# Kernel tuning notes

Measured on AMD Instinct MI355X. Metric: run time of the kernel, lower is better.

The kernel has to match this reference:

```python
import jax, jax.numpy as jnp
import numpy as np

N = 65536
APP = 1024
SP = 512
HID = 512
CARD = 16
SUB = HID // CARD  # 32


def setup_inputs() -> dict:
    key = jax.random.key(0)
    ks = jax.random.split(key, 8)
    s1 = 1.0 / np.sqrt(APP)
    s2 = 1.0 / np.sqrt(SP)
    s3 = 1.0 / np.sqrt(SUB)
    return {
        "appearance": jax.random.normal(ks[0], (N, APP), jnp.float32),
        "spatial": jax.random.normal(ks[1], (N, SP), jnp.float32),
        # Batched per-branch weights (torch Linear: y = x @ W.T + b; here stored as [in, out])
        "W1": jax.random.uniform(ks[2], (CARD, APP, SUB), jnp.float32, -s1, s1),
        "b1": jax.random.uniform(ks[3], (CARD, SUB), jnp.float32, -s1, s1),
        "W2": jax.random.uniform(ks[4], (CARD, SP, SUB), jnp.float32, -s2, s2),
        "b2": jax.random.uniform(ks[5], (CARD, SP if False else SUB), jnp.float32, -s2, s2),
        "W3": jax.random.uniform(ks[6], (CARD, SUB, HID), jnp.float32, -s3, s3),
        "b3": jax.random.uniform(ks[7], (CARD, HID), jnp.float32, -s3, s3),
    }


def reference(appearance, spatial, W1, b1, W2, b2, W3, b3):
    # fc1[c] = appearance @ W1[c] + b1[c]; fc2[c] = spatial @ W2[c] + b2[c]
    h1 = jnp.einsum('na,cas->ncs', appearance, W1) + b1[None]  # [N, C, SUB]
    h2 = jnp.einsum('np,cps->ncs', spatial, W2) + b2[None]     # [N, C, SUB]
    h = jax.nn.relu(h1 + h2)
    # sum over branches of (h[:,c] @ W3[c] + b3[c]) == einsum + sum of biases
    out = jnp.einsum('ncs,csh->nh', h, W3) + jnp.sum(b3, axis=0)[None]  # [N, HID]
    return jax.nn.relu(out)
```

## Files before the change

### kernel.cpp

```cpp
#include <hip/hip_runtime.h>

typedef __attribute__((ext_vector_type(4))) float floatx4;
typedef __attribute__((ext_vector_type(8))) short bf16x8;

__device__ __forceinline__ unsigned short f2bf(float f) {
    union { float f; unsigned u; } v; v.f = f;
    unsigned r = v.u + 0x7fffu + ((v.u >> 16) & 1u);
    return (unsigned short)(r >> 16);
}

__global__ void prep_kernel(const float* __restrict__ W1, const float* __restrict__ b1,
                            const float* __restrict__ W2, const float* __restrict__ b2,
                            const float* __restrict__ W3, const float* __restrict__ b3,
                            unsigned short* __restrict__ wcat, unsigned short* __restrict__ w3f,
                            float* __restrict__ bias12, float* __restrict__ bias3s)
{
    int tid = blockIdx.x * 256 + threadIdx.x;
    if (tid < 98304) {
        int l  = tid & 63;
        int nt = (tid >> 6) & 31;
        int kc = tid >> 11;
        int n  = nt * 16 + (l & 15);
        int k0 = kc * 32 + ((l >> 4) << 3);
        int c = n >> 5, s = n & 31;
        union { unsigned short us[8]; int4 v; } pk;
        const float* src = (k0 < 1024) ? (W1 + c * 32768 + k0 * 32 + s)
                                       : (W2 + c * 16384 + (k0 - 1024) * 32 + s);
        #pragma unroll
        for (int j = 0; j < 8; ++j) pk.us[j] = f2bf(src[j * 32]);
        *(int4*)(wcat + (size_t)tid * 8) = pk.v;
    } else if (tid < 131072) {
        int t  = tid - 98304;
        int l  = t & 63;
        int nt = (t >> 6) & 31;
        int kc = t >> 11;
        int n  = nt * 16 + (l & 15);
        int k0 = kc * 32 + ((l >> 4) << 3);
        union { unsigned short us[8]; int4 v; } pk;
        const float* src = W3 + k0 * 512 + n;
        #pragma unroll
        for (int j = 0; j < 8; ++j) pk.us[j] = f2bf(src[j * 512]);
        *(int4*)(w3f + (size_t)t * 8) = pk.v;
    } else if (tid < 131584) {
        int n = tid - 131072;
        bias12[n] = b1[n] + b2[n];
        float sacc = 0.f;
        #pragma unroll
        for (int c = 0; c < 16; ++c) sacc += b3[c * 512 + n];
        bias3s[n] = sacc;
    }
}

__global__ __launch_bounds__(512, 4) void fused_main(
    const float* __restrict__ app, const float* __restrict__ sp,
    const unsigned short* __restrict__ wcat, const unsigned short* __restrict__ w3f,
    const float* __restrict__ bias12, const float* __restrict__ bias3s,
    float* __restrict__ out)
{
    __shared__ unsigned short As[2][4][64][8];
    __shared__ unsigned short Hf[4][16][64][8];

    const int tid = (int)threadIdx.x;
    const int w   = tid >> 6;
    const int l   = tid & 63;
    const int rowbase = (int)blockIdx.x * 64;

    const int sr  = tid >> 3;
    const int scc = tid & 7;
    const float* appsrc = app + (size_t)(rowbase + sr) * 1024 + scc * 4;
    const float* spsrc  = sp  + (size_t)(rowbase + sr) * 512  + scc * 4;
    unsigned short* as0 = &As[0][sr >> 4][(scc >> 1) * 16 + (sr & 15)][(scc & 1) * 4];
    unsigned short* as1 = &As[1][sr >> 4][(scc >> 1) * 16 + (sr & 15)][(scc & 1) * 4];

    floatx4 acc[4][4];
    #pragma unroll
    for (int mt = 0; mt < 4; ++mt)
        #pragma unroll
        for (int nt = 0; nt < 4; ++nt)
            acc[mt][nt] = (floatx4){0.f, 0.f, 0.f, 0.f};

    {
        float4 p = *(const float4*)(appsrc);
        union { unsigned short us[4]; int2 v; } pk;
        pk.us[0] = f2bf(p.x); pk.us[1] = f2bf(p.y);
        pk.us[2] = f2bf(p.z); pk.us[3] = f2bf(p.w);
        *(int2*)as0 = pk.v;
    }
    float4 pA = *(const float4*)(appsrc + 32);

    const unsigned short* wbase = wcat + (size_t)w * 2048 + (size_t)l * 8;
    bf16x8 bcur[4];
    #pragma unroll
    for (int nt = 0; nt < 4; ++nt)
        bcur[nt] = *(const bf16x8*)(wbase + nt * 512);

    asm volatile("s_waitcnt lgkmcnt(0)" ::: "memory");
    __builtin_amdgcn_s_barrier();
    asm volatile("" ::: "memory");

    for (int kb = 0; kb < 48; ++kb) {
        bf16x8 af[4];
        #pragma unroll
        for (int mt = 0; mt < 4; ++mt)
            af[mt] = *(const bf16x8*)(&As[kb & 1][mt][l][0]);

        float4 pB;
        if (kb + 2 < 48) {
            const float* src = (kb + 2 < 32) ? (appsrc + (kb + 2) * 32)
                                             : (spsrc + (kb - 30) * 32);
            pB = *(const float4*)src;
        }

        if (kb + 1 < 48) {
            union { unsigned short us[4]; int2 v; } pk;
            pk.us[0] = f2bf(pA.x); pk.us[1] = f2bf(pA.y);
            pk.us[2] = f2bf(pA.z); pk.us[3] = f2bf(pA.w);
            *(int2*)(((kb & 1) == 0) ? as1 : as0) = pk.v;
        }

        const unsigned short* wp = wbase + (size_t)(kb + 1) * 16384;
        #pragma unroll
        for (int nt = 0; nt < 4; ++nt) {
            #pragma unroll
            for (int mt = 0; mt < 4; ++mt)
                acc[mt][nt] = __builtin_amdgcn_mfma_f32_16x16x32_bf16(
                    af[mt], bcur[nt], acc[mt][nt], 0, 0, 0);
            if (kb + 1 < 48)
                bcur[nt] = *(const bf16x8*)(wp + nt * 512);
        }

        pA = pB;

        if (kb + 1 < 48) {
            asm volatile("s_waitcnt lgkmcnt(0)" ::: "memory");
            __builtin_amdgcn_s_barrier();
            asm volatile("" ::: "memory");
        }
    }

    const unsigned short* w3base = w3f + (size_t)w * 2048 + (size_t)l * 8;
    bf16x8 b3[4];
    #pragma unroll
    for (int nt = 0; nt < 4; ++nt)
        b3[nt] = *(const bf16x8*)(w3base + nt * 512);

    #pragma unroll
    for (int nt = 0; nt < 4; ++nt) {
        const int colg = w * 64 + nt * 16 + (l & 15);
        const float bv = bias12[colg];
        const int kc  = colg >> 5;
        const int lhi = ((colg >> 3) & 3) << 4;
        const int j   = colg & 7;
        #pragma unroll
        for (int mt = 0; mt < 4; ++mt)
            #pragma unroll
            for (int r = 0; r < 4; ++r) {
                const int rlow = ((l >> 4) << 2) + r;
                float v = acc[mt][nt][r] + bv;
                v = fmaxf(v, 0.f);
                Hf[mt][kc][lhi + rlow][j] = f2bf(v);
            }
    }
    asm volatile("s_waitcnt lgkmcnt(0)" ::: "memory");
    __builtin_amdgcn_s_barrier();
    asm volatile("" ::: "memory");

    #pragma unroll
    for (int mt = 0; mt < 4; ++mt)
        #pragma unroll
        for (int nt = 0; nt < 4; ++nt)
            acc[mt][nt] = (floatx4){0.f, 0.f, 0.f, 0.f};

    for (int kc = 0; kc < 16; ++kc) {
        bf16x8 af[4];
        #pragma unroll
        for (int mt = 0; mt < 4; ++mt)
            af[mt] = *(const bf16x8*)(&Hf[mt][kc][l][0]);
        const unsigned short* wp = w3base + (size_t)(kc + 1) * 16384;
        #pragma unroll
        for (int nt = 0; nt < 4; ++nt) {
            #pragma unroll
            for (int mt = 0; mt < 4; ++mt)
                acc[mt][nt] = __builtin_amdgcn_mfma_f32_16x16x32_bf16(
                    af[mt], b3[nt], acc[mt][nt], 0, 0, 0);
            if (kc + 1 < 16)
                b3[nt] = *(const bf16x8*)(wp + nt * 512);
        }
    }

    #pragma unroll
    for (int nt = 0; nt < 4; ++nt) {
        const int colg = w * 64 + nt * 16 + (l & 15);
        const float bv = bias3s[colg];
        #pragma unroll
        for (int mt = 0; mt < 4; ++mt)
            #pragma unroll
            for (int r = 0; r < 4; ++r) {
                const int rowg = mt * 16 + ((l >> 4) << 2) + r;
                float v = acc[mt][nt][r] + bv;
                v = fmaxf(v, 0.f);
                out[(size_t)(rowbase + rowg) * 512 + colg] = v;
            }
    }
}

extern "C" void kernel_launch(void* const* d_in, const int* in_sizes, int n_in,
                              void* d_out, int out_size, void* d_ws, size_t ws_size,
                              hipStream_t stream)
{
    const float* app = (const float*)d_in[0];
    const float* sp  = (const float*)d_in[1];
    const float* W1  = (const float*)d_in[2];
    const float* b1  = (const float*)d_in[3];
    const float* W2  = (const float*)d_in[4];
    const float* b2  = (const float*)d_in[5];
    const float* W3  = (const float*)d_in[6];
    const float* b3  = (const float*)d_in[7];

    char* ws = (char*)d_ws;
    unsigned short* wcat  = (unsigned short*)(ws);
    unsigned short* w3f   = (unsigned short*)(ws + 1572864);
    float*          b12   = (float*)(ws + 2097152);
    float*          b3s   = (float*)(ws + 2099200);

    prep_kernel<<<514, 256, 0, stream>>>(W1, b1, W2, b2, W3, b3, wcat, w3f, b12, b3s);

    float* outp = (float*)d_out;
    fused_main<<<65536 / 64, 512, 0, stream>>>(app, sp, wcat, w3f, b12, b3s, outp);
}
```

Before: 581.6 us.

## Double K-step per barrier, overlay LDS buffers, add MFMA priority hints

The main GEMM loop now handles 64 K elements per iteration instead of 32. This halves the number of block barriers, and each thread loads 8 floats per row chunk with 128-bit LDS stores. The A staging buffer and the hidden-activation buffer now share LDS through a union, which lowers the shared-memory footprint per block. Weight fragments are loaded for two K-steps at once into 8 registers, and s_setprio raises wave priority around the MFMA bursts in both GEMMs. The cost is higher register pressure and a shallower prefetch distance for the activation loads, now one iteration ahead.

```diff
diff --git a/kernel.cpp b/kernel.cpp
--- a/kernel.cpp
+++ b/kernel.cpp
@@ -57,20 +57,22 @@
     const float* __restrict__ bias12, const float* __restrict__ bias3s,
     float* __restrict__ out)
 {
-    __shared__ unsigned short As[2][4][64][8];
-    __shared__ unsigned short Hf[4][16][64][8];
+    __shared__ union {
+        unsigned short As[2][2][4][64][8];
+        unsigned short Hf[4][16][64][8];
+    } sh;
 
     const int tid = (int)threadIdx.x;
     const int w   = tid >> 6;
     const int l   = tid & 63;
     const int rowbase = (int)blockIdx.x * 64;
 
-    const int sr  = tid >> 3;
-    const int scc = tid & 7;
-    const float* appsrc = app + (size_t)(rowbase + sr) * 1024 + scc * 4;
-    const float* spsrc  = sp  + (size_t)(rowbase + sr) * 512  + scc * 4;
-    unsigned short* as0 = &As[0][sr >> 4][(scc >> 1) * 16 + (sr & 15)][(scc & 1) * 4];
-    unsigned short* as1 = &As[1][sr >> 4][(scc >> 1) * 16 + (sr & 15)][(scc & 1) * 4];
+    const int sr = tid >> 3;
+    const int kq = tid & 7;
+    const float* appsrc = app + (size_t)(rowbase + sr) * 1024 + kq * 8;
+    const float* spsrc  = sp  + (size_t)(rowbase + sr) * 512  + kq * 8;
+    unsigned short* as0 = &sh.As[0][kq >> 2][sr >> 4][(kq & 3) * 16 + (sr & 15)][0];
+    unsigned short* as1 = &sh.As[1][kq >> 2][sr >> 4][(kq & 3) * 16 + (sr & 15)][0];
 
     floatx4 acc[4][4];
     #pragma unroll
@@ -79,70 +81,79 @@
         for (int nt = 0; nt < 4; ++nt)
             acc[mt][nt] = (floatx4){0.f, 0.f, 0.f, 0.f};
 
+    const unsigned short* wbase = wcat + (size_t)w * 2048 + (size_t)l * 8;
+
+    bf16x8 bcur[8];
+    #pragma unroll
+    for (int i = 0; i < 8; ++i)
+        bcur[i] = *(const bf16x8*)(wbase + (i >> 2) * 16384 + (i & 3) * 512);
     {
-        float4 p = *(const float4*)(appsrc);
-        union { unsigned short us[4]; int2 v; } pk;
-        pk.us[0] = f2bf(p.x); pk.us[1] = f2bf(p.y);
-        pk.us[2] = f2bf(p.z); pk.us[3] = f2bf(p.w);
-        *(int2*)as0 = pk.v;
-    }
-    float4 pA = *(const float4*)(appsrc + 32);
-
-    const unsigned short* wbase = wcat + (size_t)w * 2048 + (size_t)l * 8;
-    bf16x8 bcur[4];
-    #pragma unroll
-    for (int nt = 0; nt < 4; ++nt)
-        bcur[nt] = *(const bf16x8*)(wbase + nt * 512);
-
+        float4 q0 = *(const float4*)(appsrc);
+        float4 q1 = *(const float4*)(appsrc + 4);
+        union { unsigned short us[8]; int4 v; } pk;
+        pk.us[0] = f2bf(q0.x); pk.us[1] = f2bf(q0.y); pk.us[2] = f2bf(q0.z); pk.us[3] = f2bf(q0.w);
+        pk.us[4] = f2bf(q1.x); pk.us[5] = f2bf(q1.y); pk.us[6] = f2bf(q1.z); pk.us[7] = f2bf(q1.w);
+        *(int4*)as0 = pk.v;
+    }
     asm volatile("s_waitcnt lgkmcnt(0)" ::: "memory");
     __builtin_amdgcn_s_barrier();
-    asm volatile("" ::: "memory");
-
-    for (int kb = 0; kb < 48; ++kb) {
+
+    for (int p = 0; p < 24; ++p) {
+        const int buf = p & 1;
+        unsigned short* dst = buf ? as0 : as1;
+
+        float4 pA0, pA1;
+        if (p + 1 < 24) {
+            const float* src = (p + 1 < 16) ? (appsrc + (p + 1) * 64)
+                                            : (spsrc + (p - 15) * 64);
+            pA0 = *(const float4*)src;
+            pA1 = *(const float4*)(src + 4);
+        }
+
         bf16x8 af[4];
         #pragma unroll
         for (int mt = 0; mt < 4; ++mt)
-            af[mt] = *(const bf16x8*)(&As[kb & 1][mt][l][0]);
-
-        float4 pB;
-        if (kb + 2 < 48) {
-            const float* src = (kb + 2 < 32) ? (appsrc + (kb + 2) * 32)
-                                             : (spsrc + (kb - 30) * 32);
-            pB = *(const float4*)src;
+            af[mt] = *(const bf16x8*)(&sh.As[buf][0][mt][l][0]);
+        __builtin_amdgcn_s_setprio(1);
+        #pragma unroll
+        for (int mt = 0; mt < 4; ++mt)
+            #pragma unroll
+            for (int nt = 0; nt < 4; ++nt)
+                acc[mt][nt] = __builtin_amdgcn_mfma_f32_16x16x32_bf16(
+                    af[mt], bcur[nt], acc[mt][nt], 0, 0, 0);
+        __builtin_amdgcn_s_setprio(0);
+        #pragma unroll
+        for (int mt = 0; mt < 4; ++mt)
+            af[mt] = *(const bf16x8*)(&sh.As[buf][1][mt][l][0]);
+        __builtin_amdgcn_s_setprio(1);
+        #pragma unroll
+        for (int mt = 0; mt < 4; ++mt)
+            #pragma unroll
+            for (int nt = 0; nt < 4; ++nt)
+                acc[mt][nt] = __builtin_amdgcn_mfma_f32_16x16x32_bf16(
+                    af[mt], bcur[4 + nt], acc[mt][nt], 0, 0, 0);
+        __builtin_amdgcn_s_setprio(0);
+
+        if (p + 1 < 24) {
+            const unsigned short* wp = wbase + (size_t)(p + 1) * 32768;
+            #pragma unroll
+            for (int i = 0; i < 8; ++i)
+                bcur[i] = *(const bf16x8*)(wp + (i >> 2) * 16384 + (i & 3) * 512);
+            union { unsigned short us[8]; int4 v; } pk;
+            pk.us[0] = f2bf(pA0.x); pk.us[1] = f2bf(pA0.y); pk.us[2] = f2bf(pA0.z); pk.us[3] = f2bf(pA0.w);
+            pk.us[4] = f2bf(pA1.x); pk.us[5] = f2bf(pA1.y); pk.us[6] = f2bf(pA1.z); pk.us[7] = f2bf(pA1.w);
+            *(int4*)dst = pk.v;
         }
 
-        if (kb + 1 < 48) {
-            union { unsigned short us[4]; int2 v; } pk;
-            pk.us[0] = f2bf(pA.x); pk.us[1] = f2bf(pA.y);
-            pk.us[2] = f2bf(pA.z); pk.us[3] = f2bf(pA.w);
-            *(int2*)(((kb & 1) == 0) ? as1 : as0) = pk.v;
-        }
-
-        const unsigned short* wp = wbase + (size_t)(kb + 1) * 16384;
-        #pragma unroll
-        for (int nt = 0; nt < 4; ++nt) {
-            #pragma unroll
-            for (int mt = 0; mt < 4; ++mt)
-                acc[mt][nt] = __builtin_amdgcn_mfma_f32_16x16x32_bf16(
-                    af[mt], bcur[nt], acc[mt][nt], 0, 0, 0);
-            if (kb + 1 < 48)
-                bcur[nt] = *(const bf16x8*)(wp + nt * 512);
-        }
-
-        pA = pB;
-
-        if (kb + 1 < 48) {
-            asm volatile("s_waitcnt lgkmcnt(0)" ::: "memory");
-            __builtin_amdgcn_s_barrier();
-            asm volatile("" ::: "memory");
-        }
+        asm volatile("s_waitcnt lgkmcnt(0)" ::: "memory");
+        __builtin_amdgcn_s_barrier();
     }
 
     const unsigned short* w3base = w3f + (size_t)w * 2048 + (size_t)l * 8;
-    bf16x8 b3[4];
-    #pragma unroll
-    for (int nt = 0; nt < 4; ++nt)
-        b3[nt] = *(const bf16x8*)(w3base + nt * 512);
+    bf16x8 b3[8];
+    #pragma unroll
+    for (int i = 0; i < 8; ++i)
+        b3[i] = *(const bf16x8*)(w3base + (i >> 2) * 16384 + (i & 3) * 512);
 
     #pragma unroll
     for (int nt = 0; nt < 4; ++nt) {
@@ -158,12 +169,11 @@
                 const int rlow = ((l >> 4) << 2) + r;
                 float v = acc[mt][nt][r] + bv;
                 v = fmaxf(v, 0.f);
-                Hf[mt][kc][lhi + rlow][j] = f2bf(v);
+                sh.Hf[mt][kc][lhi + rlow][j] = f2bf(v);
             }
     }
     asm volatile("s_waitcnt lgkmcnt(0)" ::: "memory");
     __builtin_amdgcn_s_barrier();
-    asm volatile("" ::: "memory");
 
     #pragma unroll
     for (int mt = 0; mt < 4; ++mt)
@@ -171,20 +181,35 @@
         for (int nt = 0; nt < 4; ++nt)
             acc[mt][nt] = (floatx4){0.f, 0.f, 0.f, 0.f};
 
-    for (int kc = 0; kc < 16; ++kc) {
+    for (int q = 0; q < 8; ++q) {
         bf16x8 af[4];
         #pragma unroll
         for (int mt = 0; mt < 4; ++mt)
-            af[mt] = *(const bf16x8*)(&Hf[mt][kc][l][0]);
-        const unsigned short* wp = w3base + (size_t)(kc + 1) * 16384;
-        #pragma unroll
-        for (int nt = 0; nt < 4; ++nt) {
-            #pragma unroll
-            for (int mt = 0; mt < 4; ++mt)
+            af[mt] = *(const bf16x8*)(&sh.Hf[mt][2 * q][l][0]);
+        __builtin_amdgcn_s_setprio(1);
+        #pragma unroll
+        for (int mt = 0; mt < 4; ++mt)
+            #pragma unroll
+            for (int nt = 0; nt < 4; ++nt)
                 acc[mt][nt] = __builtin_amdgcn_mfma_f32_16x16x32_bf16(
                     af[mt], b3[nt], acc[mt][nt], 0, 0, 0);
-            if (kc + 1 < 16)
-                b3[nt] = *(const bf16x8*)(wp + nt * 512);
+        __builtin_amdgcn_s_setprio(0);
+        #pragma unroll
+        for (int mt = 0; mt < 4; ++mt)
+            af[mt] = *(const bf16x8*)(&sh.Hf[mt][2 * q + 1][l][0]);
+        __builtin_amdgcn_s_setprio(1);
+        #pragma unroll
+        for (int mt = 0; mt < 4; ++mt)
+            #pragma unroll
+            for (int nt = 0; nt < 4; ++nt)
+                acc[mt][nt] = __builtin_amdgcn_mfma_f32_16x16x32_bf16(
+                    af[mt], b3[4 + nt], acc[mt][nt], 0, 0, 0);
+        __builtin_amdgcn_s_setprio(0);
+        if (q + 1 < 8) {
+            const unsigned short* wp = w3base + (size_t)(q + 1) * 32768;
+            #pragma unroll
+            for (int i = 0; i < 8; ++i)
+                b3[i] = *(const bf16x8*)(wp + (i >> 2) * 16384 + (i & 3) * 512);
         }
     }
 
```

New measurement: 542.8 us. -6.7%, faster.
